# Kernel tuning notes

Measured on AMD Instinct MI355X. Metric: run time of the kernel, lower is better.

Reference implementation:

```python
import jax, jax.numpy as jnp
import numpy as np

N = 262144
D_IN = 32
D_OUT = 32
K = 9  # 3x3 kernel offsets


def setup_inputs() -> dict:
    key = jax.random.key(0)
    k1, k2, k3, k4, k5 = jax.random.split(key, 5)
    feat = jax.random.normal(k1, (N, D_IN), dtype=jnp.float32)
    weight = jax.random.normal(k2, (D_OUT, 3, 3, D_IN), dtype=jnp.float32)
    bias = jax.random.normal(k3, (D_OUT,), dtype=jnp.float32)
    indice_pairs = jax.random.randint(k4, (2, K, N), 0, N, dtype=jnp.int32)
    indice_pair_num = jax.random.randint(k5, (K,), 0, N, dtype=jnp.int32)
    return {"feat": feat, "weight": weight, "bias": bias,
            "indice_pairs": indice_pairs, "indice_pair_num": indice_pair_num}


def reference(feat, weight, bias, indice_pairs, indice_pair_num):
    # spconv Native indice_conv: per kernel offset k, gather inputs at
    # indice_pairs[0,k,:n_k], GEMM with weight[:,k], scatter-add to
    # output rows indice_pairs[1,k,:n_k]; then add bias.
    d_out = weight.shape[0]
    w = weight.reshape(d_out, K, D_IN).transpose(1, 2, 0)  # [K, d_in, d_out]
    in_idx = indice_pairs[0]   # [K, P]
    out_idx = indice_pairs[1]  # [K, P]
    P = in_idx.shape[1]
    valid = jnp.arange(P, dtype=jnp.int32)[None, :] < indice_pair_num[:, None]  # [K, P]
    gathered = feat[in_idx]                                   # [K, P, d_in]
    gathered = jnp.where(valid[..., None], gathered, 0.0)
    contrib = jnp.einsum('kpc,kcd->kpd', gathered, w)         # [K, P, d_out]
    out = jnp.zeros((feat.shape[0], d_out), dtype=feat.dtype)
    out = out.at[out_idx.reshape(-1)].add(contrib.reshape(-1, d_out))
    return out + bias[None, :]
```

## Files before the change

kernel.cpp:

```cpp
#include <hip/hip_runtime.h>

#define KOFF 9
#define N_PTS 262144
#define D 32
#define BINS 512
#define ROWS_PER_BIN 512
#define TILE_ROWS 513
#define CAP 640
#define OVER_CAP 524288
#define SENT (512u << 18)

typedef __attribute__((ext_vector_type(4))) float f32x4;
typedef __attribute__((ext_vector_type(8))) short short8;

__device__ inline short f2bf(float f) {
    unsigned u = __float_as_uint(f);
    u = (u + 0x7fffu + ((u >> 16) & 1u)) >> 16;
    return (short)u;
}

__global__ void __launch_bounds__(256)
fill_kernel(const int* __restrict__ indice_pairs,
            const int* __restrict__ indice_pair_num,
            int* __restrict__ counts,
            unsigned int* __restrict__ buckets,
            uint2* __restrict__ overlist,
            int* __restrict__ over_n) {
    const int k = blockIdx.y;
    const int n_k = indice_pair_num[k];
    if (blockIdx.x * 256 >= n_k) return;
    const int p = blockIdx.x * 256 + threadIdx.x;
    if (p >= n_k) return;
    int irow = indice_pairs[(size_t)k * N_PTS + p];
    int orow = indice_pairs[(size_t)(KOFF + k) * N_PTS + p];
    int bin = orow >> 9, olow = orow & 511;
    int b = bin * KOFF + k;
    int slot = atomicAdd(&counts[b], 1);
    if (slot < CAP) {
        buckets[(size_t)b * CAP + slot] = (unsigned)irow | ((unsigned)olow << 18);
    } else {
        int s2 = atomicAdd(over_n, 1);
        if (s2 < OVER_CAP) overlist[s2] = make_uint2((unsigned)irow | ((unsigned)k << 18),
                                                     (unsigned)orow);
    }
}

__global__ void __launch_bounds__(512, 4)
phase2_kernel(const float* __restrict__ feat,
              const float* __restrict__ weight,
              const float* __restrict__ bias,
              const int* __restrict__ counts,
              const unsigned int* __restrict__ buckets,
              float* __restrict__ out) {
    __shared__ f32x4 tile4[TILE_ROWS * D / 4];
    float* tile = (float*)tile4;

    const int bin  = blockIdx.x;
    const int tid  = threadIdx.x;
    const int wave = tid >> 6;
    const int lane = tid & 63;

    f32x4 z = {0.f, 0.f, 0.f, 0.f};
    for (int i = tid; i < TILE_ROWS * D / 4; i += 512) tile4[i] = z;
    __syncthreads();

    const int arow = lane & 15;
    const int hoff = (lane >> 4) << 3;

#pragma unroll 1
    for (int k = 0; k < KOFF; ++k) {
        short8 bf0, bf1;
        {
            const float* wp0 = weight + (size_t)arow * (KOFF * D) + k * D + hoff;
            const float* wp1 = wp0 + 16 * (KOFF * D);
            f32x4 w0 = *(const f32x4*)wp0;
            f32x4 w1 = *(const f32x4*)(wp0 + 4);
            f32x4 w2 = *(const f32x4*)wp1;
            f32x4 w3 = *(const f32x4*)(wp1 + 4);
#pragma unroll
            for (int j = 0; j < 4; ++j) {
                bf0[j] = f2bf(w0[j]); bf0[j + 4] = f2bf(w1[j]);
                bf1[j] = f2bf(w2[j]); bf1[j + 4] = f2bf(w3[j]);
            }
        }

        int cnt = counts[bin * KOFF + k];
        cnt = cnt < CAP ? cnt : CAP;
        const unsigned* bk = buckets + (size_t)(bin * KOFF + k) * CAP;
        int ngroups = (cnt + 15) >> 4;

        unsigned entA = SENT; f32x4 fa0 = z, fa1 = z;
        int g = wave;
        if (g < ngroups) {
            int ei = g * 16 + arow;
            entA = (ei < cnt) ? bk[ei] : SENT;
            const float* fp = feat + ((size_t)(entA & 0x3ffff) << 5) + hoff;
            fa0 = *(const f32x4*)fp; fa1 = *(const f32x4*)(fp + 4);
        }
#pragma unroll 1
        for (; g < ngroups; g += 8) {
            unsigned entB = SENT; f32x4 fb0 = z, fb1 = z;
            int gn = g + 8;
            if (gn < ngroups) {
                int ei = gn * 16 + arow;
                entB = (ei < cnt) ? bk[ei] : SENT;
                const float* fp = feat + ((size_t)(entB & 0x3ffff) << 5) + hoff;
                fb0 = *(const f32x4*)fp; fb1 = *(const f32x4*)(fp + 4);
            }

            short8 af;
#pragma unroll
            for (int j = 0; j < 4; ++j) { af[j] = f2bf(fa0[j]); af[j + 4] = f2bf(fa1[j]); }

            f32x4 acc0 = __builtin_amdgcn_mfma_f32_16x16x32_bf16(af, bf0, z, 0, 0, 0);
            f32x4 acc1 = __builtin_amdgcn_mfma_f32_16x16x32_bf16(af, bf1, z, 0, 0, 0);

#pragma unroll
            for (int rg = 0; rg < 4; ++rg) {
                int crow = ((lane >> 4) << 2) + rg;
                int entc = __builtin_amdgcn_ds_bpermute(crow << 2, (int)entA);
                int rl   = ((unsigned)entc >> 18) & 0x3ff;
                int sw   = ((rl >> 2) & 1) << 4;
                float* t = &tile[rl * D + (arow ^ sw)];
                atomicAdd(t, acc0[rg]);
                atomicAdd(&tile[rl * D + ((arow + 16) ^ sw)], acc1[rg]);
            }
            entA = entB; fa0 = fb0; fa1 = fb1;
        }
    }
    __syncthreads();

    f32x4 b4 = ((const f32x4*)bias)[tid & 7];
    for (int i = tid; i < ROWS_PER_BIN * 8; i += 512) {
        int row = i >> 3, c4 = i & 7;
        int sc4 = c4 ^ (((row >> 2) & 1) << 2);
        f32x4 v = tile4[row * 8 + sc4];
        v += b4;
        *(f32x4*)&out[((size_t)(bin * ROWS_PER_BIN + row)) * D + c4 * 4] = v;
    }
}

__global__ void overflow_kernel(const float* __restrict__ feat,
                                const float* __restrict__ weight,
                                const uint2* __restrict__ overlist,
                                const int* __restrict__ over_n,
                                float* __restrict__ out) {
    int n = *over_n;
    n = n < OVER_CAP ? n : OVER_CAP;
    for (int i = blockIdx.x * blockDim.x + threadIdx.x; i < n;
         i += gridDim.x * blockDim.x) {
        uint2 e = overlist[i];
        int irow = e.x & 0x3ffff, k = (e.x >> 18) & 15, orow = (int)e.y;
        float fr[D];
#pragma unroll
        for (int c = 0; c < D; c += 4)
            *(f32x4*)&fr[c] = *(const f32x4*)&feat[(size_t)irow * D + c];
#pragma unroll 1
        for (int dd = 0; dd < D; ++dd) {
            float a = 0.f;
#pragma unroll
            for (int c = 0; c < D; ++c)
                a += fr[c] * weight[dd * (KOFF * D) + k * D + c];
            atomicAdd(&out[(size_t)orow * D + dd], a);
        }
    }
}

__global__ void bias_init_kernel(const float* __restrict__ bias,
                                 float* __restrict__ out) {
    int i = blockIdx.x * blockDim.x + threadIdx.x;
    float4 b = ((const float4*)bias)[i & 7];
    ((float4*)out)[i] = b;
}

#define PPB 8
__global__ void __launch_bounds__(256)
scatter_conv_kernel(const float* __restrict__ feat,
                    const float* __restrict__ weight,
                    const int* __restrict__ indice_pairs,
                    const int* __restrict__ indice_pair_num,
                    float* __restrict__ out) {
    const int k   = blockIdx.y;
    const int n_k = indice_pair_num[k];
    const int p0  = blockIdx.x * PPB;
    if (p0 >= n_k) return;
    __shared__ float w[D][D];
    __shared__ float f[PPB][D];
    for (int idx = threadIdx.x; idx < D * D; idx += 256) {
        int c = idx >> 5, d = idx & 31;
        w[c][d] = weight[d * (KOFF * D) + k * D + c];
    }
    const int pp = threadIdx.x >> 5;
    const int d  = threadIdx.x & 31;
    const int p  = p0 + pp;
    int orow = -1;
    if (p < n_k) {
        int irow = indice_pairs[(size_t)k * N_PTS + p];
        orow     = indice_pairs[(size_t)(KOFF + k) * N_PTS + p];
        f[pp][d] = feat[(size_t)irow * D + d];
    }
    __syncthreads();
    if (p < n_k) {
        float acc = 0.f;
#pragma unroll
        for (int c = 0; c < D; ++c) acc += f[pp][c] * w[c][d];
        atomicAdd(&out[(size_t)orow * D + d], acc);
    }
}

extern "C" void kernel_launch(void* const* d_in, const int* in_sizes, int n_in,
                              void* d_out, int out_size, void* d_ws, size_t ws_size,
                              hipStream_t stream) {
    const float* feat            = (const float*)d_in[0];
    const float* weight          = (const float*)d_in[1];
    const float* bias            = (const float*)d_in[2];
    const int*   indice_pairs    = (const int*)d_in[3];
    const int*   indice_pair_num = (const int*)d_in[4];
    float*       out             = (float*)d_out;

    const size_t HDR   = 32768;
    const size_t BKT   = (size_t)BINS * KOFF * CAP * 4;
    const size_t OVERB = (size_t)OVER_CAP * 8;
    const size_t need  = HDR + BKT + OVERB;

    if (ws_size >= need) {
        int*          counts   = (int*)d_ws;
        int*          over_n   = (int*)((char*)d_ws + 20480);
        unsigned int* buckets  = (unsigned int*)((char*)d_ws + HDR);
        uint2*        overlist = (uint2*)((char*)d_ws + HDR + BKT);

        hipMemsetAsync(d_ws, 0, HDR, stream);
        dim3 fgrid(N_PTS / 256, KOFF);
        fill_kernel<<<fgrid, 256, 0, stream>>>(indice_pairs, indice_pair_num,
                                               counts, buckets, overlist, over_n);
        phase2_kernel<<<BINS, 512, 0, stream>>>(feat, weight, bias, counts,
                                                buckets, out);
        overflow_kernel<<<64, 256, 0, stream>>>(feat, weight, overlist, over_n, out);
    } else {
        int n_vec4 = N_PTS * D / 4;
        bias_init_kernel<<<n_vec4 / 256, 256, 0, stream>>>(bias, out);
        dim3 grid((N_PTS + PPB - 1) / PPB, KOFF);
        scatter_conv_kernel<<<grid, 256, 0, stream>>>(
            feat, weight, indice_pairs, indice_pair_num, out);
    }
}
```

Measured before the change: 351.2 us.

## Split bucket counters per XCD and process fixed segments per wave with 1024 threads

The fill kernel now reads the XCC id and keeps separate counters and sub-buckets for each of the 8 XCDs, so the global atomics no longer contend across dies. Phase 2 runs 1024 threads per bin. Each of the 16 waves takes a fixed range of the 72 (offset, XCD) segments, loads up to 5 groups of 16 entries at once and prefetches the next segment's entries. The risk is overflow: a sub-bucket holds only 80 entries and the overflow list is now smaller, so more points may take the slow atomic path. Entries past 80 per segment that were dropped from the list would be lost.

```diff
diff --git a/kernel.cpp b/kernel.cpp
--- a/kernel.cpp
+++ b/kernel.cpp
@@ -6,8 +6,10 @@
 #define BINS 512
 #define ROWS_PER_BIN 512
 #define TILE_ROWS 513
-#define CAP 640
-#define OVER_CAP 524288
+#define NXCD 8
+#define SUBCAP 80
+#define NSEG (KOFF * NXCD)
+#define OVER_CAP 131072
 #define SENT (512u << 18)
 
 typedef __attribute__((ext_vector_type(4))) float f32x4;
@@ -31,13 +33,18 @@
     if (blockIdx.x * 256 >= n_k) return;
     const int p = blockIdx.x * 256 + threadIdx.x;
     if (p >= n_k) return;
+
+    unsigned xcd;
+    asm volatile("s_getreg_b32 %0, hwreg(HW_REG_XCC_ID)" : "=s"(xcd));
+    xcd &= 7;
+
     int irow = indice_pairs[(size_t)k * N_PTS + p];
     int orow = indice_pairs[(size_t)(KOFF + k) * N_PTS + p];
     int bin = orow >> 9, olow = orow & 511;
-    int b = bin * KOFF + k;
-    int slot = atomicAdd(&counts[b], 1);
-    if (slot < CAP) {
-        buckets[(size_t)b * CAP + slot] = (unsigned)irow | ((unsigned)olow << 18);
+    int idx = (int)xcd * (BINS * KOFF) + bin * KOFF + k;
+    int slot = atomicAdd(&counts[idx], 1);
+    if (slot < SUBCAP) {
+        buckets[(size_t)idx * SUBCAP + slot] = (unsigned)irow | ((unsigned)olow << 18);
     } else {
         int s2 = atomicAdd(over_n, 1);
         if (s2 < OVER_CAP) overlist[s2] = make_uint2((unsigned)irow | ((unsigned)k << 18),
@@ -45,7 +52,31 @@
     }
 }
 
-__global__ void __launch_bounds__(512, 4)
+#define SEG_INFO(J, CNT, BK, KV) { int s_ = start + (J); KV = s_ >> 3; int x_ = s_ & 7; \
+    int idx_ = x_ * (BINS * KOFF) + bin * KOFF + KV; \
+    CNT = counts[idx_]; CNT = CNT < SUBCAP ? CNT : SUBCAP; \
+    BK = buckets + (size_t)idx_ * SUBCAP; }
+
+#define LOAD_ENT(BK, CNT, E, G) E = ((G)*16 + arow < (CNT)) ? (BK)[(G)*16 + arow] : SENT;
+
+#define LOAD_FEAT(E, F0, F1, G, CNT) if ((G)*16 < (CNT)) { \
+    const float* fp_ = feat + ((size_t)((E) & 0x3ffff) << 5) + hoff; \
+    F0 = *(const f32x4*)fp_; F1 = *(const f32x4*)(fp_ + 4); }
+
+#define COMPUTE(E, F0, F1, G, CNT) if ((G)*16 < (CNT)) { \
+    short8 af_; \
+    _Pragma("unroll") for (int j_ = 0; j_ < 4; ++j_) { af_[j_] = f2bf(F0[j_]); af_[j_+4] = f2bf(F1[j_]); } \
+    f32x4 a0_ = __builtin_amdgcn_mfma_f32_16x16x32_bf16(af_, bfa, z, 0, 0, 0); \
+    f32x4 a1_ = __builtin_amdgcn_mfma_f32_16x16x32_bf16(af_, bfb, z, 0, 0, 0); \
+    _Pragma("unroll") for (int rg_ = 0; rg_ < 4; ++rg_) { \
+        int crow_ = ((lane >> 4) << 2) + rg_; \
+        int entc_ = __builtin_amdgcn_ds_bpermute(crow_ << 2, (int)(E)); \
+        int rl_ = ((unsigned)entc_ >> 18) & 0x3ff; \
+        int sw_ = ((rl_ >> 2) & 1) << 4; \
+        atomicAdd(&tile[rl_ * D + (arow ^ sw_)], a0_[rg_]); \
+        atomicAdd(&tile[rl_ * D + ((arow + 16) ^ sw_)], a1_[rg_]); } }
+
+__global__ void __launch_bounds__(1024, 4)
 phase2_kernel(const float* __restrict__ feat,
               const float* __restrict__ weight,
               const float* __restrict__ bias,
@@ -61,77 +92,70 @@
     const int lane = tid & 63;
 
     f32x4 z = {0.f, 0.f, 0.f, 0.f};
-    for (int i = tid; i < TILE_ROWS * D / 4; i += 512) tile4[i] = z;
+    for (int i = tid; i < TILE_ROWS * D / 4; i += 1024) tile4[i] = z;
     __syncthreads();
 
     const int arow = lane & 15;
     const int hoff = (lane >> 4) << 3;
 
+    const int start = (wave < 8) ? wave * 5 : 40 + (wave - 8) * 4;
+    const int nseg  = (wave < 8) ? 5 : 4;
+
+    int kcur, cnt_cur; const unsigned* bk_cur;
+    SEG_INFO(0, cnt_cur, bk_cur, kcur);
+    unsigned e0, e1, e2, e3, e4;
+    LOAD_ENT(bk_cur, cnt_cur, e0, 0) LOAD_ENT(bk_cur, cnt_cur, e1, 1)
+    LOAD_ENT(bk_cur, cnt_cur, e2, 2) LOAD_ENT(bk_cur, cnt_cur, e3, 3)
+    LOAD_ENT(bk_cur, cnt_cur, e4, 4)
+
+    short8 bfa = {0,0,0,0,0,0,0,0}, bfb = {0,0,0,0,0,0,0,0};
+    int kloaded = -1;
+
 #pragma unroll 1
-    for (int k = 0; k < KOFF; ++k) {
-        short8 bf0, bf1;
-        {
-            const float* wp0 = weight + (size_t)arow * (KOFF * D) + k * D + hoff;
+    for (int j = 0; j < nseg; ++j) {
+        int knext = kcur, cnt_next = 0; const unsigned* bk_next = bk_cur;
+        unsigned n0 = SENT, n1 = SENT, n2 = SENT, n3 = SENT, n4 = SENT;
+        if (j + 1 < nseg) {
+            SEG_INFO(j + 1, cnt_next, bk_next, knext);
+            LOAD_ENT(bk_next, cnt_next, n0, 0) LOAD_ENT(bk_next, cnt_next, n1, 1)
+            LOAD_ENT(bk_next, cnt_next, n2, 2) LOAD_ENT(bk_next, cnt_next, n3, 3)
+            LOAD_ENT(bk_next, cnt_next, n4, 4)
+        }
+
+        if (kloaded != kcur) {
+            const float* wp0 = weight + (size_t)arow * (KOFF * D) + kcur * D + hoff;
             const float* wp1 = wp0 + 16 * (KOFF * D);
-            f32x4 w0 = *(const f32x4*)wp0;
-            f32x4 w1 = *(const f32x4*)(wp0 + 4);
-            f32x4 w2 = *(const f32x4*)wp1;
-            f32x4 w3 = *(const f32x4*)(wp1 + 4);
-#pragma unroll
-            for (int j = 0; j < 4; ++j) {
-                bf0[j] = f2bf(w0[j]); bf0[j + 4] = f2bf(w1[j]);
-                bf1[j] = f2bf(w2[j]); bf1[j + 4] = f2bf(w3[j]);
+            f32x4 w0 = *(const f32x4*)wp0, w1 = *(const f32x4*)(wp0 + 4);
+            f32x4 w2 = *(const f32x4*)wp1, w3 = *(const f32x4*)(wp1 + 4);
+#pragma unroll
+            for (int jq = 0; jq < 4; ++jq) {
+                bfa[jq] = f2bf(w0[jq]); bfa[jq + 4] = f2bf(w1[jq]);
+                bfb[jq] = f2bf(w2[jq]); bfb[jq + 4] = f2bf(w3[jq]);
             }
+            kloaded = kcur;
         }
 
-        int cnt = counts[bin * KOFF + k];
-        cnt = cnt < CAP ? cnt : CAP;
-        const unsigned* bk = buckets + (size_t)(bin * KOFF + k) * CAP;
-        int ngroups = (cnt + 15) >> 4;
-
-        unsigned entA = SENT; f32x4 fa0 = z, fa1 = z;
-        int g = wave;
-        if (g < ngroups) {
-            int ei = g * 16 + arow;
-            entA = (ei < cnt) ? bk[ei] : SENT;
-            const float* fp = feat + ((size_t)(entA & 0x3ffff) << 5) + hoff;
-            fa0 = *(const f32x4*)fp; fa1 = *(const f32x4*)(fp + 4);
-        }
-#pragma unroll 1
-        for (; g < ngroups; g += 8) {
-            unsigned entB = SENT; f32x4 fb0 = z, fb1 = z;
-            int gn = g + 8;
-            if (gn < ngroups) {
-                int ei = gn * 16 + arow;
-                entB = (ei < cnt) ? bk[ei] : SENT;
-                const float* fp = feat + ((size_t)(entB & 0x3ffff) << 5) + hoff;
-                fb0 = *(const f32x4*)fp; fb1 = *(const f32x4*)(fp + 4);
-            }
-
-            short8 af;
-#pragma unroll
-            for (int j = 0; j < 4; ++j) { af[j] = f2bf(fa0[j]); af[j + 4] = f2bf(fa1[j]); }
-
-            f32x4 acc0 = __builtin_amdgcn_mfma_f32_16x16x32_bf16(af, bf0, z, 0, 0, 0);
-            f32x4 acc1 = __builtin_amdgcn_mfma_f32_16x16x32_bf16(af, bf1, z, 0, 0, 0);
-
-#pragma unroll
-            for (int rg = 0; rg < 4; ++rg) {
-                int crow = ((lane >> 4) << 2) + rg;
-                int entc = __builtin_amdgcn_ds_bpermute(crow << 2, (int)entA);
-                int rl   = ((unsigned)entc >> 18) & 0x3ff;
-                int sw   = ((rl >> 2) & 1) << 4;
-                float* t = &tile[rl * D + (arow ^ sw)];
-                atomicAdd(t, acc0[rg]);
-                atomicAdd(&tile[rl * D + ((arow + 16) ^ sw)], acc1[rg]);
-            }
-            entA = entB; fa0 = fb0; fa1 = fb1;
-        }
+        f32x4 fa0 = z, fa1 = z, fb0 = z, fb1 = z, fc0 = z, fc1 = z,
+              fd0 = z, fd1 = z, fe0 = z, fe1 = z;
+        LOAD_FEAT(e0, fa0, fa1, 0, cnt_cur)
+        LOAD_FEAT(e1, fb0, fb1, 1, cnt_cur)
+        LOAD_FEAT(e2, fc0, fc1, 2, cnt_cur)
+        LOAD_FEAT(e3, fd0, fd1, 3, cnt_cur)
+        LOAD_FEAT(e4, fe0, fe1, 4, cnt_cur)
+
+        COMPUTE(e0, fa0, fa1, 0, cnt_cur)
+        COMPUTE(e1, fb0, fb1, 1, cnt_cur)
+        COMPUTE(e2, fc0, fc1, 2, cnt_cur)
+        COMPUTE(e3, fd0, fd1, 3, cnt_cur)
+        COMPUTE(e4, fe0, fe1, 4, cnt_cur)
+
+        e0 = n0; e1 = n1; e2 = n2; e3 = n3; e4 = n4;
+        cnt_cur = cnt_next; bk_cur = bk_next; kcur = knext;
     }
     __syncthreads();
 
     f32x4 b4 = ((const f32x4*)bias)[tid & 7];
-    for (int i = tid; i < ROWS_PER_BIN * 8; i += 512) {
+    for (int i = tid; i < ROWS_PER_BIN * 8; i += 1024) {
         int row = i >> 3, c4 = i & 7;
         int sc4 = c4 ^ (((row >> 2) & 1) << 2);
         f32x4 v = tile4[row * 8 + sc4];
@@ -218,14 +242,15 @@
     const int*   indice_pair_num = (const int*)d_in[4];
     float*       out             = (float*)d_out;
 
-    const size_t HDR   = 32768;
-    const size_t BKT   = (size_t)BINS * KOFF * CAP * 4;
+    const size_t CNTB  = (size_t)NXCD * BINS * KOFF * 4;
+    const size_t HDR   = 151552;
+    const size_t BKT   = (size_t)NXCD * BINS * KOFF * SUBCAP * 4;
     const size_t OVERB = (size_t)OVER_CAP * 8;
     const size_t need  = HDR + BKT + OVERB;
 
     if (ws_size >= need) {
         int*          counts   = (int*)d_ws;
-        int*          over_n   = (int*)((char*)d_ws + 20480);
+        int*          over_n   = (int*)((char*)d_ws + CNTB);
         unsigned int* buckets  = (unsigned int*)((char*)d_ws + HDR);
         uint2*        overlist = (uint2*)((char*)d_ws + HDR + BKT);
 
@@ -233,8 +258,8 @@
         dim3 fgrid(N_PTS / 256, KOFF);
         fill_kernel<<<fgrid, 256, 0, stream>>>(indice_pairs, indice_pair_num,
                                                counts, buckets, overlist, over_n);
-        phase2_kernel<<<BINS, 512, 0, stream>>>(feat, weight, bias, counts,
-                                                buckets, out);
+        phase2_kernel<<<BINS, 1024, 0, stream>>>(feat, weight, bias, counts,
+                                                 buckets, out);
         overflow_kernel<<<64, 256, 0, stream>>>(feat, weight, overlist, over_n, out);
     } else {
         int n_vec4 = N_PTS * D / 4;
```

Result: slower. 388.4 us (+10.6%).

## Bucket pairs per output row and accumulate in MFMA registers

Applied to the files above, without the earlier changes.

Replaces the per-bin, per-offset bucketing with per-output-row buckets of up to 16 entries. Each row's entries are sorted by kernel offset inside the wave, and a wave of 16 rows accumulates its outputs with bf16 MFMA straight into registers, so no LDS tile and no LDS atomic scatter are needed. Bias is folded into the accumulator init, and entries beyond 16 per row go to a smaller overflow list handled by global atomics. This trades the LDS atomics for a per-output-row atomic counter pass and padded MFMA iterations, since every lane loops up to the wave's maximum count per offset.

```diff
diff --git a/kernel.cpp b/kernel.cpp
--- a/kernel.cpp
+++ b/kernel.cpp
@@ -3,12 +3,8 @@
 #define KOFF 9
 #define N_PTS 262144
 #define D 32
-#define BINS 512
-#define ROWS_PER_BIN 512
-#define TILE_ROWS 513
-#define CAP 640
-#define OVER_CAP 524288
-#define SENT (512u << 18)
+#define RCAP 16
+#define OVER_CAP 131072
 
 typedef __attribute__((ext_vector_type(4))) float f32x4;
 typedef __attribute__((ext_vector_type(8))) short short8;
@@ -20,12 +16,12 @@
 }
 
 __global__ void __launch_bounds__(256)
-fill_kernel(const int* __restrict__ indice_pairs,
-            const int* __restrict__ indice_pair_num,
-            int* __restrict__ counts,
-            unsigned int* __restrict__ buckets,
-            uint2* __restrict__ overlist,
-            int* __restrict__ over_n) {
+fill_row_kernel(const int* __restrict__ indice_pairs,
+                const int* __restrict__ indice_pair_num,
+                int* __restrict__ counts,
+                unsigned int* __restrict__ buckets,
+                uint2* __restrict__ overlist,
+                int* __restrict__ over_n) {
     const int k = blockIdx.y;
     const int n_k = indice_pair_num[k];
     if (blockIdx.x * 256 >= n_k) return;
@@ -33,110 +29,130 @@
     if (p >= n_k) return;
     int irow = indice_pairs[(size_t)k * N_PTS + p];
     int orow = indice_pairs[(size_t)(KOFF + k) * N_PTS + p];
-    int bin = orow >> 9, olow = orow & 511;
-    int b = bin * KOFF + k;
-    int slot = atomicAdd(&counts[b], 1);
-    if (slot < CAP) {
-        buckets[(size_t)b * CAP + slot] = (unsigned)irow | ((unsigned)olow << 18);
+    unsigned ent = ((unsigned)k << 18) | (unsigned)irow;
+    int slot = atomicAdd(&counts[orow], 1);
+    if (slot < RCAP) {
+        buckets[(size_t)orow * RCAP + slot] = ent;
     } else {
         int s2 = atomicAdd(over_n, 1);
-        if (s2 < OVER_CAP) overlist[s2] = make_uint2((unsigned)irow | ((unsigned)k << 18),
-                                                     (unsigned)orow);
-    }
-}
-
-__global__ void __launch_bounds__(512, 4)
-phase2_kernel(const float* __restrict__ feat,
-              const float* __restrict__ weight,
-              const float* __restrict__ bias,
-              const int* __restrict__ counts,
-              const unsigned int* __restrict__ buckets,
-              float* __restrict__ out) {
-    __shared__ f32x4 tile4[TILE_ROWS * D / 4];
-    float* tile = (float*)tile4;
-
-    const int bin  = blockIdx.x;
+        if (s2 < OVER_CAP) overlist[s2] = make_uint2(ent, (unsigned)orow);
+    }
+}
+
+__global__ void __launch_bounds__(512)
+rowgemm_kernel(const float* __restrict__ feat,
+               const float* __restrict__ weight,
+               const float* __restrict__ bias,
+               const int* __restrict__ counts,
+               const unsigned int* __restrict__ buckets,
+               float* __restrict__ out) {
+    __shared__ unsigned slds[8 * 16 * RCAP];
     const int tid  = threadIdx.x;
     const int wave = tid >> 6;
     const int lane = tid & 63;
-
-    f32x4 z = {0.f, 0.f, 0.f, 0.f};
-    for (int i = tid; i < TILE_ROWS * D / 4; i += 512) tile4[i] = z;
-    __syncthreads();
-
-    const int arow = lane & 15;
-    const int hoff = (lane >> 4) << 3;
-
+    const int c    = lane >> 4;
+    const int s    = lane & 15;
+    const int hoff = c << 3;
+    const int r0   = blockIdx.x * 128 + wave * 16;
+    const int r    = r0 + s;
+
+    int cnt = counts[r];
+    cnt = cnt < RCAP ? cnt : RCAP;
+
+    unsigned e[16];
+    {
+        const uint4* b4 = (const uint4*)(buckets + (size_t)r * RCAP);
+        uint4 q0 = b4[0], q1 = b4[1], q2 = b4[2], q3 = b4[3];
+        e[0]=q0.x; e[1]=q0.y; e[2]=q0.z; e[3]=q0.w;
+        e[4]=q1.x; e[5]=q1.y; e[6]=q1.z; e[7]=q1.w;
+        e[8]=q2.x; e[9]=q2.y; e[10]=q2.z; e[11]=q2.w;
+        e[12]=q3.x; e[13]=q3.y; e[14]=q3.z; e[15]=q3.w;
+    }
+#pragma unroll
+    for (int i = 0; i < 16; ++i)
+        if (i >= cnt) e[i] = 0xFFFFFFFFu;
+
+    unsigned ky[16];
+#pragma unroll
+    for (int i = 0; i < 16; ++i) ky[i] = e[i] >> 18;
+
+    unsigned* myrow = slds + wave * 256 + s * 16;
+#pragma unroll
+    for (int i = 0; i < 16; ++i) {
+        int pos = 0;
+#pragma unroll
+        for (int j = 0; j < 16; ++j) {
+            if (j < i)      pos += (ky[j] <= ky[i]);
+            else if (j > i) pos += (ky[j] <  ky[i]);
+        }
+        if (c == 0) myrow[pos] = e[i];
+    }
+
+    int offs[10];
+    offs[0] = 0;
+#pragma unroll
+    for (int k = 1; k <= 9; ++k) {
+        int o = 0;
+#pragma unroll
+        for (int i = 0; i < 16; ++i) o += (ky[i] < (unsigned)k);
+        offs[k] = o;
+    }
+
+    float b0 = bias[s], b1 = bias[s + 16];
+    f32x4 acc0 = {b0, b0, b0, b0};
+    f32x4 acc1 = {b1, b1, b1, b1};
+    const short8 z8 = {0, 0, 0, 0, 0, 0, 0, 0};
+
+#pragma unroll
+    for (int k = 0; k < KOFF; ++k) {
+        int ckl = offs[k + 1] - offs[k];
+        int m = ckl;
+#pragma unroll
+        for (int d = 1; d < 64; d <<= 1) {
+            int t = __shfl_xor(m, d);
+            m = m > t ? m : t;
+        }
+        if (m > 0) {
+            const float* wp0 = weight + (size_t)s * (KOFF * D) + k * D + hoff;
+            const float* wp1 = wp0 + 16 * (KOFF * D);
+            f32x4 w0 = *(const f32x4*)wp0, w1 = *(const f32x4*)(wp0 + 4);
+            f32x4 w2 = *(const f32x4*)wp1, w3 = *(const f32x4*)(wp1 + 4);
+            short8 bfa, bfb;
+#pragma unroll
+            for (int j = 0; j < 4; ++j) {
+                bfa[j] = f2bf(w0[j]); bfa[j + 4] = f2bf(w1[j]);
+                bfb[j] = f2bf(w2[j]); bfb[j + 4] = f2bf(w3[j]);
+            }
+
+            const int p0i = offs[k];
+            unsigned entA = myrow[p0i & 15];
+            int irA = entA & 0x3ffff;
+            const float* fpA = feat + (size_t)irA * D + hoff;
+            f32x4 fa0 = *(const f32x4*)fpA, fa1 = *(const f32x4*)(fpA + 4);
 #pragma unroll 1
-    for (int k = 0; k < KOFF; ++k) {
-        short8 bf0, bf1;
-        {
-            const float* wp0 = weight + (size_t)arow * (KOFF * D) + k * D + hoff;
-            const float* wp1 = wp0 + 16 * (KOFF * D);
-            f32x4 w0 = *(const f32x4*)wp0;
-            f32x4 w1 = *(const f32x4*)(wp0 + 4);
-            f32x4 w2 = *(const f32x4*)wp1;
-            f32x4 w3 = *(const f32x4*)(wp1 + 4);
-#pragma unroll
-            for (int j = 0; j < 4; ++j) {
-                bf0[j] = f2bf(w0[j]); bf0[j + 4] = f2bf(w1[j]);
-                bf1[j] = f2bf(w2[j]); bf1[j + 4] = f2bf(w3[j]);
+            for (int i = 0; i < m; ++i) {
+                unsigned entB = myrow[(p0i + i + 1) & 15];
+                int irB = entB & 0x3ffff;
+                const float* fpB = feat + (size_t)irB * D + hoff;
+                f32x4 fb0 = *(const f32x4*)fpB, fb1 = *(const f32x4*)(fpB + 4);
+
+                short8 af;
+#pragma unroll
+                for (int j = 0; j < 4; ++j) { af[j] = f2bf(fa0[j]); af[j + 4] = f2bf(fa1[j]); }
+                if (i >= ckl) af = z8;
+
+                acc0 = __builtin_amdgcn_mfma_f32_16x16x32_bf16(af, bfa, acc0, 0, 0, 0);
+                acc1 = __builtin_amdgcn_mfma_f32_16x16x32_bf16(af, bfb, acc1, 0, 0, 0);
+                entA = entB; fa0 = fb0; fa1 = fb1;
             }
         }
-
-        int cnt = counts[bin * KOFF + k];
-        cnt = cnt < CAP ? cnt : CAP;
-        const unsigned* bk = buckets + (size_t)(bin * KOFF + k) * CAP;
-        int ngroups = (cnt + 15) >> 4;
-
-        unsigned entA = SENT; f32x4 fa0 = z, fa1 = z;
-        int g = wave;
-        if (g < ngroups) {
-            int ei = g * 16 + arow;
-            entA = (ei < cnt) ? bk[ei] : SENT;
-            const float* fp = feat + ((size_t)(entA & 0x3ffff) << 5) + hoff;
-            fa0 = *(const f32x4*)fp; fa1 = *(const f32x4*)(fp + 4);
-        }
-#pragma unroll 1
-        for (; g < ngroups; g += 8) {
-            unsigned entB = SENT; f32x4 fb0 = z, fb1 = z;
-            int gn = g + 8;
-            if (gn < ngroups) {
-                int ei = gn * 16 + arow;
-                entB = (ei < cnt) ? bk[ei] : SENT;
-                const float* fp = feat + ((size_t)(entB & 0x3ffff) << 5) + hoff;
-                fb0 = *(const f32x4*)fp; fb1 = *(const f32x4*)(fp + 4);
-            }
-
-            short8 af;
-#pragma unroll
-            for (int j = 0; j < 4; ++j) { af[j] = f2bf(fa0[j]); af[j + 4] = f2bf(fa1[j]); }
-
-            f32x4 acc0 = __builtin_amdgcn_mfma_f32_16x16x32_bf16(af, bf0, z, 0, 0, 0);
-            f32x4 acc1 = __builtin_amdgcn_mfma_f32_16x16x32_bf16(af, bf1, z, 0, 0, 0);
-
-#pragma unroll
-            for (int rg = 0; rg < 4; ++rg) {
-                int crow = ((lane >> 4) << 2) + rg;
-                int entc = __builtin_amdgcn_ds_bpermute(crow << 2, (int)entA);
-                int rl   = ((unsigned)entc >> 18) & 0x3ff;
-                int sw   = ((rl >> 2) & 1) << 4;
-                float* t = &tile[rl * D + (arow ^ sw)];
-                atomicAdd(t, acc0[rg]);
-                atomicAdd(&tile[rl * D + ((arow + 16) ^ sw)], acc1[rg]);
-            }
-            entA = entB; fa0 = fb0; fa1 = fb1;
-        }
-    }
-    __syncthreads();
-
-    f32x4 b4 = ((const f32x4*)bias)[tid & 7];
-    for (int i = tid; i < ROWS_PER_BIN * 8; i += 512) {
-        int row = i >> 3, c4 = i & 7;
-        int sc4 = c4 ^ (((row >> 2) & 1) << 2);
-        f32x4 v = tile4[row * 8 + sc4];
-        v += b4;
-        *(f32x4*)&out[((size_t)(bin * ROWS_PER_BIN + row)) * D + c4 * 4] = v;
+    }
+
+#pragma unroll
+    for (int g = 0; g < 4; ++g) {
+        int row = r0 + c * 4 + g;
+        out[(size_t)row * D + s]      = acc0[g];
+        out[(size_t)row * D + s + 16] = acc1[g];
     }
 }
 
@@ -149,19 +165,19 @@
     n = n < OVER_CAP ? n : OVER_CAP;
     for (int i = blockIdx.x * blockDim.x + threadIdx.x; i < n;
          i += gridDim.x * blockDim.x) {
-        uint2 e = overlist[i];
-        int irow = e.x & 0x3ffff, k = (e.x >> 18) & 15, orow = (int)e.y;
+        uint2 ev = overlist[i];
+        int irow = ev.x & 0x3ffff, k = (ev.x >> 18) & 15, orow = (int)ev.y;
         float fr[D];
 #pragma unroll
-        for (int c = 0; c < D; c += 4)
-            *(f32x4*)&fr[c] = *(const f32x4*)&feat[(size_t)irow * D + c];
+        for (int ch = 0; ch < D; ch += 4)
+            *(f32x4*)&fr[ch] = *(const f32x4*)&feat[(size_t)irow * D + ch];
 #pragma unroll 1
         for (int dd = 0; dd < D; ++dd) {
             float a = 0.f;
 #pragma unroll
-            for (int c = 0; c < D; ++c)
-                a += fr[c] * weight[dd * (KOFF * D) + k * D + c];
-            atomicAdd(&out[(size_t)orow * D + dd], a);
+            for (int ch = 0; ch < D; ++ch)
+                a += fr[ch] * weight[dd * (KOFF * D) + k * D + ch];
+            unsafeAtomicAdd(&out[(size_t)orow * D + dd], a);
         }
     }
 }
@@ -187,8 +203,8 @@
     __shared__ float w[D][D];
     __shared__ float f[PPB][D];
     for (int idx = threadIdx.x; idx < D * D; idx += 256) {
-        int c = idx >> 5, d = idx & 31;
-        w[c][d] = weight[d * (KOFF * D) + k * D + c];
+        int ch = idx >> 5, d = idx & 31;
+        w[ch][d] = weight[d * (KOFF * D) + k * D + ch];
     }
     const int pp = threadIdx.x >> 5;
     const int d  = threadIdx.x & 31;
@@ -203,8 +219,8 @@
     if (p < n_k) {
         float acc = 0.f;
 #pragma unroll
-        for (int c = 0; c < D; ++c) acc += f[pp][c] * w[c][d];
-        atomicAdd(&out[(size_t)orow * D + d], acc);
+        for (int ch = 0; ch < D; ++ch) acc += f[pp][ch] * w[ch][d];
+        unsafeAtomicAdd(&out[(size_t)orow * D + d], acc);
     }
 }
 
@@ -218,23 +234,24 @@
     const int*   indice_pair_num = (const int*)d_in[4];
     float*       out             = (float*)d_out;
 
-    const size_t HDR   = 32768;
-    const size_t BKT   = (size_t)BINS * KOFF * CAP * 4;
+    const size_t CNTB  = (size_t)N_PTS * 4;
+    const size_t HDR   = CNTB + 4096;
+    const size_t BKT   = (size_t)N_PTS * RCAP * 4;
     const size_t OVERB = (size_t)OVER_CAP * 8;
     const size_t need  = HDR + BKT + OVERB;
 
     if (ws_size >= need) {
-        int*          counts   = (int*)d_ws;
-        int*          over_n   = (int*)((char*)d_ws + 20480);
+        int*          cnts     = (int*)d_ws;
+        int*          over_n   = (int*)((char*)d_ws + CNTB);
         unsigned int* buckets  = (unsigned int*)((char*)d_ws + HDR);
         uint2*        overlist = (uint2*)((char*)d_ws + HDR + BKT);
 
         hipMemsetAsync(d_ws, 0, HDR, stream);
         dim3 fgrid(N_PTS / 256, KOFF);
-        fill_kernel<<<fgrid, 256, 0, stream>>>(indice_pairs, indice_pair_num,
-                                               counts, buckets, overlist, over_n);
-        phase2_kernel<<<BINS, 512, 0, stream>>>(feat, weight, bias, counts,
-                                                buckets, out);
+        fill_row_kernel<<<fgrid, 256, 0, stream>>>(indice_pairs, indice_pair_num,
+                                                   cnts, buckets, overlist, over_n);
+        rowgemm_kernel<<<N_PTS / 128, 512, 0, stream>>>(feat, weight, bias,
+                                                        cnts, buckets, out);
         overflow_kernel<<<64, 256, 0, stream>>>(feat, weight, overlist, over_n, out);
     } else {
         int n_vec4 = N_PTS * D / 4;
```

Result: faster. 314.1 us (-10.6%).
